# Optimization experiments

Measured on AMD Instinct MI355X. Metric: run time of the kernel, lower is better.

The kernel has to match this reference:

```python
import jax, jax.numpy as jnp
import numpy as np
from jax import lax

B, T, D, L = 64, 512, 1024, 32


def setup_inputs() -> dict:
    key = jax.random.key(0)
    ks = jax.random.split(key, 6)
    embeddings = jax.random.normal(ks[0], (B, T, D), dtype=jnp.float32)
    W = jax.random.normal(ks[1], (L, D), dtype=jnp.float32) * (1.0 / np.sqrt(D))
    b = jnp.zeros((L,), dtype=jnp.float32)
    start_trans = jax.random.normal(ks[2], (L,), dtype=jnp.float32) * 0.1
    end_trans = jax.random.normal(ks[3], (L,), dtype=jnp.float32) * 0.1
    trans = jax.random.normal(ks[4], (L, L), dtype=jnp.float32) * 0.1
    labels = jax.random.randint(ks[5], (B, T), 0, L, dtype=jnp.int32)
    mask = jnp.ones((B, T), dtype=bool)  # torchcrf requires mask[:, 0] == True
    return {"embeddings": embeddings, "W": W, "b": b,
            "start_trans": start_trans, "end_trans": end_trans,
            "trans": trans, "labels": labels, "mask": mask}


def _crf_nll(emissions, labels, mask, start_trans, end_trans, trans):
    # emissions: [B, T, L]; torchcrf works time-first internally.
    em = jnp.transpose(emissions, (1, 0, 2))          # [T, B, L]
    tg = labels.T                                      # [T, B]
    mk_b = mask.T                                      # [T, B] bool
    mk_f = mk_b.astype(emissions.dtype)
    bidx = jnp.arange(em.shape[1])

    # ---- numerator: score of the gold tag path ----
    score0 = start_trans[tg[0]] + em[0, bidx, tg[0]]   # [B]

    def num_step(carry, inp):
        prev_tag, score = carry
        e_t, tag_t, m_b, m_f = inp
        step = trans[prev_tag, tag_t] + e_t[bidx, tag_t]
        score = score + step * m_f
        prev_tag = jnp.where(m_b, tag_t, prev_tag)
        return (prev_tag, score), None

    (last_tag, num), _ = lax.scan(num_step, (tg[0], score0),
                                  (em[1:], tg[1:], mk_b[1:], mk_f[1:]))
    num = num + end_trans[last_tag]

    # ---- denominator: forward algorithm (log partition) ----
    alpha0 = start_trans[None, :] + em[0]              # [B, L]

    def den_step(alpha, inp):
        e_t, m_b = inp
        # alpha[b, i] + trans[i, j] + e_t[b, j] -> logsumexp over i
        nxt = jax.nn.logsumexp(alpha[:, :, None] + trans[None, :, :]
                               + e_t[:, None, :], axis=1)
        alpha = jnp.where(m_b[:, None], nxt, alpha)
        return alpha, None

    alpha, _ = lax.scan(den_step, alpha0, (em[1:], mk_b[1:]))
    den = jax.nn.logsumexp(alpha + end_trans[None, :], axis=1)  # [B]

    llh = num - den                                    # log-likelihood per seq
    return -jnp.mean(llh)                              # reduction='mean', negated


def reference(embeddings, W, b, start_trans, end_trans, trans, labels, mask):
    # dropout is identity at eval time
    emissions = jnp.einsum('btd,ld->btl', embeddings, W) + b  # [B, T, L]
    return _crf_nll(emissions, labels, mask, start_trans, end_trans, trans)
```

## Files before the change

kernel.cpp:

```cpp
#include <hip/hip_runtime.h>
#include <hip/hip_bf16.h>

#define NB 64
#define NT 512
#define ND 1024
#define NL 32
#define SEG 16
#define NSEG 32

typedef __attribute__((ext_vector_type(8)))  short bf16x8;
typedef __attribute__((ext_vector_type(4)))  float f32x4;
typedef __attribute__((ext_vector_type(16))) float f32x16;

__device__ __forceinline__ unsigned short bfh(float x) {
    __hip_bfloat16 h = __float2bfloat16(x);
    return *(unsigned short*)&h;
}
__device__ __forceinline__ float frombf(unsigned short u) {
    return __uint_as_float(((unsigned)u) << 16);
}
__device__ __forceinline__ bf16x8 pack8(float4 x, float4 y) {
    bf16x8 r;
    unsigned short* p = (unsigned short*)&r;
    p[0] = bfh(x.x); p[1] = bfh(x.y); p[2] = bfh(x.z); p[3] = bfh(x.w);
    p[4] = bfh(y.x); p[5] = bfh(y.y); p[6] = bfh(y.z); p[7] = bfh(y.w);
    return r;
}

__global__ __launch_bounds__(256) void wb_kernel(
    const float* __restrict__ W, unsigned short* __restrict__ Wb)
{
    int i = blockIdx.x * 256 + threadIdx.x;
    float4 v = ((const float4*)W)[i];
    ushort4 o;
    o.x = bfh(v.x); o.y = bfh(v.y); o.z = bfh(v.z); o.w = bfh(v.w);
    ((ushort4*)Wb)[i] = o;
}

struct Grp {
    float4 a[4][2];
    bf16x8 b[4][2];
};

__device__ __forceinline__ void load_grp(
    Grp& G, const float* __restrict__ ap,
    const unsigned short* __restrict__ bp0,
    const unsigned short* __restrict__ bp1, int k0)
{
#pragma unroll
    for (int s = 0; s < 4; s++) {
        G.a[s][0] = *(const float4*)(ap + k0 + s * 32);
        G.a[s][1] = *(const float4*)(ap + k0 + s * 32 + 4);
        G.b[s][0] = *(const bf16x8*)(bp0 + k0 + s * 32);
        G.b[s][1] = *(const bf16x8*)(bp1 + k0 + s * 32);
    }
}

__global__ __launch_bounds__(256) void emis_kernel(
    const float* __restrict__ emb,
    const unsigned short* __restrict__ Wb,
    const float* __restrict__ bias,
    float* __restrict__ eme)
{
    const int tid  = threadIdx.x;
    const int wv   = tid >> 6;
    const int lane = tid & 63;
    const int m    = lane & 15;
    const int quad = lane >> 4;
    const int w    = blockIdx.x * 4 + wv;
    const int row  = w * 16 + m;

    const float*          ap  = emb + (size_t)row * ND + quad * 8;
    const unsigned short* bp0 = Wb + (size_t)m * ND + quad * 8;
    const unsigned short* bp1 = Wb + (size_t)(16 + m) * ND + quad * 8;

    f32x4 acc0 = {0.f, 0.f, 0.f, 0.f};
    f32x4 acc1 = {0.f, 0.f, 0.f, 0.f};

    Grp g0, g1;
    load_grp(g0, ap, bp0, bp1, 0);
    load_grp(g1, ap, bp0, bp1, 128);

#pragma unroll
    for (int g = 0; g < 8; g++) {
        Grp& cur = (g & 1) ? g1 : g0;
#pragma unroll
        for (int s = 0; s < 4; s++) {
            bf16x8 af = pack8(cur.a[s][0], cur.a[s][1]);
            acc0 = __builtin_amdgcn_mfma_f32_16x16x32_bf16(af, cur.b[s][0], acc0, 0, 0, 0);
            acc1 = __builtin_amdgcn_mfma_f32_16x16x32_bf16(af, cur.b[s][1], acc1, 0, 0, 0);
        }
        if (g < 6) load_grp(cur, ap, bp0, bp1, (g + 2) * 128);
    }

    const float bl0 = bias[m];
    const float bl1 = bias[16 + m];
#pragma unroll
    for (int r = 0; r < 4; r++) {
        int R = w * 16 + quad * 4 + r;
        float* op = eme + (size_t)R * NL;
        op[m]      = __expf(acc0[r] + bl0);
        op[16 + m] = __expf(acc1[r] + bl1);
    }
}

__global__ __launch_bounds__(64) void seg_kernel(
    const float* __restrict__ eme,
    const float* __restrict__ trans,
    const int*   __restrict__ labels,
    float* __restrict__ Pm,
    int*   __restrict__ exps,
    float* __restrict__ numpart)
{
    const int blk  = blockIdx.x;
    const int b    = blk >> 5;
    const int s    = blk & 31;
    const int lane = threadIdx.x;
    const int col  = lane & 31;
    const int h    = lane >> 5;
    const int t0   = s * SEG;
    const int tstart = (s == 0) ? 1 : t0;

    __shared__ __align__(16) float em_lds[SEG][NL];
    __shared__ __align__(16) unsigned short Thi[2][32][40];
    __shared__ __align__(16) unsigned short Tlo[2][32][40];

    {
        const float* src = eme + ((size_t)b * NT + t0) * NL;
        *(float4*)&((float*)em_lds)[lane * 8]     = *(const float4*)&src[lane * 8];
        *(float4*)&((float*)em_lds)[lane * 8 + 4] = *(const float4*)&src[lane * 8 + 4];
    }
    __syncthreads();

    {
        float npart = 0.f;
        if (lane < SEG) {
            int t = t0 + lane;
            if (t >= 1) {
                int pt = labels[b * NT + t - 1], ct = labels[b * NT + t];
                npart = trans[pt * NL + ct] + __logf(em_lds[lane][ct]);
            }
        }
#pragma unroll
        for (int mk = 32; mk >= 1; mk >>= 1) npart += __shfl_xor(npart, mk, 64);
        if (lane == 0) numpart[b * NSEG + s] = npart;
    }

    float Ecol[16];
#pragma unroll
    for (int j = 0; j < 8; j++) Ecol[j]     = __expf(trans[(8 * h + j) * NL + col]);
#pragma unroll
    for (int j = 0; j < 8; j++) Ecol[8 + j] = __expf(trans[(16 + 8 * h + j) * NL + col]);

    bf16x8 Ah1, Ah2, Al1, Al2;
    {
        const float* emt = em_lds[tstart - t0];
#pragma unroll
        for (int j = 0; j < 8; j++) {
            int k1 = 8 * h + j, k2 = 16 + 8 * h + j;
            float v1 = __expf(trans[col * NL + k1]) * emt[k1];
            float v2 = __expf(trans[col * NL + k2]) * emt[k2];
            unsigned short h1 = bfh(v1), h2 = bfh(v2);
            ((unsigned short*)&Ah1)[j] = h1;
            ((unsigned short*)&Ah2)[j] = h2;
            ((unsigned short*)&Al1)[j] = bfh(v1 - frombf(h1));
            ((unsigned short*)&Al2)[j] = bfh(v2 - frombf(h2));
        }
    }

    int eseg = 0, par = 0;
    const int tlast = t0 + SEG - 1;
    for (int t = tstart + 1; t <= tlast; t++) {
        float emn = em_lds[t - t0][col];
        bf16x8 Bh1, Bh2, Bl1, Bl2;
#pragma unroll
        for (int j = 0; j < 8; j++) {
            float v1 = Ecol[j] * emn;
            float v2 = Ecol[8 + j] * emn;
            unsigned short h1 = bfh(v1), h2 = bfh(v2);
            ((unsigned short*)&Bh1)[j] = h1;
            ((unsigned short*)&Bh2)[j] = h2;
            ((unsigned short*)&Bl1)[j] = bfh(v1 - frombf(h1));
            ((unsigned short*)&Bl2)[j] = bfh(v2 - frombf(h2));
        }

        f32x16 acc;
#pragma unroll
        for (int i = 0; i < 16; i++) acc[i] = 0.f;
        acc = __builtin_amdgcn_mfma_f32_32x32x16_bf16(Ah1, Bh1, acc, 0, 0, 0);
        acc = __builtin_amdgcn_mfma_f32_32x32x16_bf16(Ah2, Bh2, acc, 0, 0, 0);
        acc = __builtin_amdgcn_mfma_f32_32x32x16_bf16(Ah1, Bl1, acc, 0, 0, 0);
        acc = __builtin_amdgcn_mfma_f32_32x32x16_bf16(Ah2, Bl2, acc, 0, 0, 0);
        acc = __builtin_amdgcn_mfma_f32_32x32x16_bf16(Al1, Bh1, acc, 0, 0, 0);
        acc = __builtin_amdgcn_mfma_f32_32x32x16_bf16(Al2, Bh2, acc, 0, 0, 0);

        int bits = __builtin_amdgcn_readlane(__float_as_int(acc[0]), 0);
        int e = (bits >> 23) & 255;
        eseg += e - 127;
        float scale = __uint_as_float((unsigned)(254 - e) << 23);

        if (t < tlast) {
#pragma unroll
            for (int r = 0; r < 16; r++) {
                int row = (r & 3) + 8 * (r >> 2) + 4 * h;
                float v = acc[r] * scale;
                unsigned short hi = bfh(v);
                Thi[par][row][col] = hi;
                Tlo[par][row][col] = bfh(v - frombf(hi));
            }
            __syncthreads();
            Ah1 = *(const bf16x8*)&Thi[par][col][8 * h];
            Ah2 = *(const bf16x8*)&Thi[par][col][16 + 8 * h];
            Al1 = *(const bf16x8*)&Tlo[par][col][8 * h];
            Al2 = *(const bf16x8*)&Tlo[par][col][16 + 8 * h];
            par ^= 1;
        } else {
            float* dst = Pm + ((size_t)(b * NSEG + s) << 10);
#pragma unroll
            for (int r = 0; r < 16; r++) {
                int row = (r & 3) + 8 * (r >> 2) + 4 * h;
                dst[row * 32 + col] = acc[r] * scale;
            }
        }
    }
    if (lane == 0) exps[b * NSEG + s] = eseg;
}

__global__ __launch_bounds__(64) void comb_kernel(
    const float* __restrict__ eme,
    const float* __restrict__ start_trans,
    const float* __restrict__ end_trans,
    const float* __restrict__ Pm,
    const int*   __restrict__ exps,
    const float* __restrict__ numpart,
    const int*   __restrict__ labels,
    float* __restrict__ den_out,
    float* __restrict__ num_out)
{
    const int b    = blockIdx.x;
    const int lane = threadIdx.x;
    const int col  = lane & 31;

    float a = __expf(start_trans[col]) * eme[(size_t)b * NT * NL + col];
    int sexp = 0;
    float sv[32];
#pragma unroll
    for (int i = 0; i < 32; i++)
        sv[i] = __int_as_float(__builtin_amdgcn_readlane(__float_as_int(a), i));

    const float* Pb = Pm + ((size_t)b * NSEG << 10);
    float Pc[32];
#pragma unroll
    for (int i = 0; i < 32; i++) Pc[i] = Pb[i * 32 + col];

    for (int s = 0; s < NSEG; s++) {
        float nb[32];
        if (s + 1 < NSEG) {
            const float* q = Pb + ((s + 1) << 10);
#pragma unroll
            for (int i = 0; i < 32; i++) nb[i] = q[i * 32 + col];
        } else {
#pragma unroll
            for (int i = 0; i < 32; i++) nb[i] = 0.f;
        }

        float p0 = sv[0] * Pc[0], p1 = sv[1] * Pc[1];
        float p2 = sv[2] * Pc[2], p3 = sv[3] * Pc[3];
        float p4 = sv[4] * Pc[4], p5 = sv[5] * Pc[5];
        float p6 = sv[6] * Pc[6], p7 = sv[7] * Pc[7];
#pragma unroll
        for (int i = 8; i < 32; i += 8) {
            p0 = fmaf(sv[i + 0], Pc[i + 0], p0);
            p1 = fmaf(sv[i + 1], Pc[i + 1], p1);
            p2 = fmaf(sv[i + 2], Pc[i + 2], p2);
            p3 = fmaf(sv[i + 3], Pc[i + 3], p3);
            p4 = fmaf(sv[i + 4], Pc[i + 4], p4);
            p5 = fmaf(sv[i + 5], Pc[i + 5], p5);
            p6 = fmaf(sv[i + 6], Pc[i + 6], p6);
            p7 = fmaf(sv[i + 7], Pc[i + 7], p7);
        }
        a = (((p0 + p1) + (p2 + p3)) + ((p4 + p5) + (p6 + p7)));

        int bits = __builtin_amdgcn_readlane(__float_as_int(a), 0);
        int e = (bits >> 23) & 255;
        sexp += e - 127;
        a *= __uint_as_float((unsigned)(254 - e) << 23);

#pragma unroll
        for (int i = 0; i < 32; i++)
            sv[i] = __int_as_float(__builtin_amdgcn_readlane(__float_as_int(a), i));
#pragma unroll
        for (int i = 0; i < 32; i++) Pc[i] = nb[i];
    }

    float sege = (lane < NSEG) ? (float)exps[b * NSEG + lane] : 0.f;
#pragma unroll
    for (int mk = 32; mk >= 1; mk >>= 1) sege += __shfl_xor(sege, mk, 64);

    float x = a * __expf(end_trans[col]);
#pragma unroll
    for (int mk = 16; mk >= 1; mk >>= 1) x += __shfl_xor(x, mk, 32);

    float nsum = (lane < NSEG) ? numpart[b * NSEG + lane] : 0.f;
#pragma unroll
    for (int mk = 32; mk >= 1; mk >>= 1) nsum += __shfl_xor(nsum, mk, 64);

    if (lane == 0) {
        int l0 = labels[b * NT], lT = labels[b * NT + NT - 1];
        num_out[b] = nsum + start_trans[l0]
                   + __logf(eme[(size_t)b * NT * NL + l0]) + end_trans[lT];
        den_out[b] = __logf(x)
                   + 0.69314718055994531f * ((float)sexp + sege);
    }
}

__global__ __launch_bounds__(64) void fin_kernel(
    const float* __restrict__ den, const float* __restrict__ num,
    float* __restrict__ out)
{
    int lane = threadIdx.x;
    float v = den[lane] - num[lane];
#pragma unroll
    for (int mk = 32; mk >= 1; mk >>= 1) v += __shfl_xor(v, mk, 64);
    if (lane == 0) out[0] = v * (1.0f / 64.0f);
}

extern "C" void kernel_launch(void* const* d_in, const int* in_sizes, int n_in,
                              void* d_out, int out_size, void* d_ws, size_t ws_size,
                              hipStream_t stream)
{
    const float* emb    = (const float*)d_in[0];
    const float* W      = (const float*)d_in[1];
    const float* bias   = (const float*)d_in[2];
    const float* st     = (const float*)d_in[3];
    const float* en     = (const float*)d_in[4];
    const float* tr     = (const float*)d_in[5];
    const int*   labels = (const int*)d_in[6];

    char* p = (char*)d_ws;
    float* eme = (float*)p;                  p += (size_t)NB * NT * NL * 4;
    float* Pm  = (float*)p;                  p += (size_t)NB * NSEG * 1024 * 4;
    int*   exps = (int*)p;                   p += NB * NSEG * 4;
    float* nump = (float*)p;                 p += NB * NSEG * 4;
    float* den  = (float*)p;                 p += NB * 4;
    float* num  = (float*)p;                 p += NB * 4;
    unsigned short* Wb = (unsigned short*)p;
    float* out = (float*)d_out;

    wb_kernel  <<<(NL * ND) / 1024, 256, 0, stream>>>(W, Wb);
    emis_kernel<<<(NB * NT) / 64, 256, 0, stream>>>(emb, Wb, bias, eme);
    seg_kernel <<<NB * NSEG, 64, 0, stream>>>(eme, tr, labels, Pm, exps, nump);
    comb_kernel<<<NB, 64, 0, stream>>>(eme, st, en, Pm, exps, nump, labels, den, num);
    fin_kernel <<<1, 64, 0, stream>>>(den, num, out);
}
```

Baseline: 253.0 us.

## Fuse emission GEMM with per-segment CRF transfer-matrix kernel via per-wave LDS

Merges the emission projection kernel and the segment transfer-matrix kernel, so each wave's 16 emission rows (one segment of 16 timesteps) stay in LDS instead of going through global memory. The start-transition term is folded into segment 0's initial matrix, and the combine kernel now starts from a ones vector. Block-level barriers are replaced with per-wave lgkmcnt waits because each wave owns its own LDS slices. This removes one launch and the global round trip of the emissions. The cost is that the seg work now runs with fewer, larger blocks and more LDS per block.

Result: faster. 236.1 us (-6.7%).

```diff
diff --git a/kernel.cpp b/kernel.cpp
--- a/kernel.cpp
+++ b/kernel.cpp
@@ -56,19 +56,31 @@
     }
 }
 
-__global__ __launch_bounds__(256) void emis_kernel(
+__global__ __launch_bounds__(256) void emseg_kernel(
     const float* __restrict__ emb,
     const unsigned short* __restrict__ Wb,
     const float* __restrict__ bias,
-    float* __restrict__ eme)
-{
+    const float* __restrict__ start_trans,
+    const float* __restrict__ trans,
+    const int*   __restrict__ labels,
+    float* __restrict__ Pm,
+    int*   __restrict__ exps,
+    float* __restrict__ numpart)
+{
+    __shared__ float          em_s[4][SEG][36];
+    __shared__ unsigned short Thi_s[4][32][40];
+    __shared__ unsigned short Tlo_s[4][32][40];
+
     const int tid  = threadIdx.x;
     const int wv   = tid >> 6;
     const int lane = tid & 63;
     const int m    = lane & 15;
     const int quad = lane >> 4;
     const int w    = blockIdx.x * 4 + wv;
+    const int b    = w >> 5;
+    const int s    = w & 31;
     const int row  = w * 16 + m;
+    const int t0   = s * SEG;
 
     const float*          ap  = emb + (size_t)row * ND + quad * 8;
     const unsigned short* bp0 = Wb + (size_t)m * ND + quad * 8;
@@ -85,10 +97,10 @@
     for (int g = 0; g < 8; g++) {
         Grp& cur = (g & 1) ? g1 : g0;
 #pragma unroll
-        for (int s = 0; s < 4; s++) {
-            bf16x8 af = pack8(cur.a[s][0], cur.a[s][1]);
-            acc0 = __builtin_amdgcn_mfma_f32_16x16x32_bf16(af, cur.b[s][0], acc0, 0, 0, 0);
-            acc1 = __builtin_amdgcn_mfma_f32_16x16x32_bf16(af, cur.b[s][1], acc1, 0, 0, 0);
+        for (int st = 0; st < 4; st++) {
+            bf16x8 af = pack8(cur.a[st][0], cur.a[st][1]);
+            acc0 = __builtin_amdgcn_mfma_f32_16x16x32_bf16(af, cur.b[st][0], acc0, 0, 0, 0);
+            acc1 = __builtin_amdgcn_mfma_f32_16x16x32_bf16(af, cur.b[st][1], acc1, 0, 0, 0);
         }
         if (g < 6) load_grp(cur, ap, bp0, bp1, (g + 2) * 128);
     }
@@ -97,48 +109,23 @@
     const float bl1 = bias[16 + m];
 #pragma unroll
     for (int r = 0; r < 4; r++) {
-        int R = w * 16 + quad * 4 + r;
-        float* op = eme + (size_t)R * NL;
-        op[m]      = __expf(acc0[r] + bl0);
-        op[16 + m] = __expf(acc1[r] + bl1);
-    }
-}
-
-__global__ __launch_bounds__(64) void seg_kernel(
-    const float* __restrict__ eme,
-    const float* __restrict__ trans,
-    const int*   __restrict__ labels,
-    float* __restrict__ Pm,
-    int*   __restrict__ exps,
-    float* __restrict__ numpart)
-{
-    const int blk  = blockIdx.x;
-    const int b    = blk >> 5;
-    const int s    = blk & 31;
-    const int lane = threadIdx.x;
-    const int col  = lane & 31;
-    const int h    = lane >> 5;
-    const int t0   = s * SEG;
-    const int tstart = (s == 0) ? 1 : t0;
-
-    __shared__ __align__(16) float em_lds[SEG][NL];
-    __shared__ __align__(16) unsigned short Thi[2][32][40];
-    __shared__ __align__(16) unsigned short Tlo[2][32][40];
+        int lt = quad * 4 + r;
+        em_s[wv][lt][m]      = __expf(acc0[r] + bl0);
+        em_s[wv][lt][16 + m] = __expf(acc1[r] + bl1);
+    }
+    asm volatile("s_waitcnt lgkmcnt(0)" ::: "memory");
 
     {
-        const float* src = eme + ((size_t)b * NT + t0) * NL;
-        *(float4*)&((float*)em_lds)[lane * 8]     = *(const float4*)&src[lane * 8];
-        *(float4*)&((float*)em_lds)[lane * 8 + 4] = *(const float4*)&src[lane * 8 + 4];
-    }
-    __syncthreads();
-
-    {
+        const int* lab = labels + b * NT;
         float npart = 0.f;
         if (lane < SEG) {
             int t = t0 + lane;
             if (t >= 1) {
-                int pt = labels[b * NT + t - 1], ct = labels[b * NT + t];
-                npart = trans[pt * NL + ct] + __logf(em_lds[lane][ct]);
+                int pt = lab[t - 1], ct = lab[t];
+                npart = trans[pt * NL + ct] + __logf(em_s[wv][lane][ct]);
+            } else {
+                int c0 = lab[0];
+                npart = start_trans[c0] + __logf(em_s[wv][0][c0]);
             }
         }
 #pragma unroll
@@ -146,6 +133,10 @@
         if (lane == 0) numpart[b * NSEG + s] = npart;
     }
 
+    const int col = lane & 31;
+    const int h   = lane >> 5;
+    const int ls  = (s == 0) ? 1 : 0;
+
     float Ecol[16];
 #pragma unroll
     for (int j = 0; j < 8; j++) Ecol[j]     = __expf(trans[(8 * h + j) * NL + col]);
@@ -154,12 +145,13 @@
 
     bf16x8 Ah1, Ah2, Al1, Al2;
     {
-        const float* emt = em_lds[tstart - t0];
+        float sA = 1.f;
+        if (s == 0) sA = __expf(start_trans[col]) * em_s[wv][0][col];
 #pragma unroll
         for (int j = 0; j < 8; j++) {
             int k1 = 8 * h + j, k2 = 16 + 8 * h + j;
-            float v1 = __expf(trans[col * NL + k1]) * emt[k1];
-            float v2 = __expf(trans[col * NL + k2]) * emt[k2];
+            float v1 = sA * __expf(trans[col * NL + k1]) * em_s[wv][ls][k1];
+            float v2 = sA * __expf(trans[col * NL + k2]) * em_s[wv][ls][k2];
             unsigned short h1 = bfh(v1), h2 = bfh(v2);
             ((unsigned short*)&Ah1)[j] = h1;
             ((unsigned short*)&Ah2)[j] = h2;
@@ -168,10 +160,9 @@
         }
     }
 
-    int eseg = 0, par = 0;
-    const int tlast = t0 + SEG - 1;
-    for (int t = tstart + 1; t <= tlast; t++) {
-        float emn = em_lds[t - t0][col];
+    int eseg = 0;
+    for (int lt = ls + 1; lt < SEG; lt++) {
+        float emn = em_s[wv][lt][col];
         bf16x8 Bh1, Bh2, Bl1, Bl2;
 #pragma unroll
         for (int j = 0; j < 8; j++) {
@@ -199,27 +190,26 @@
         eseg += e - 127;
         float scale = __uint_as_float((unsigned)(254 - e) << 23);
 
-        if (t < tlast) {
+        if (lt < SEG - 1) {
 #pragma unroll
             for (int r = 0; r < 16; r++) {
-                int row = (r & 3) + 8 * (r >> 2) + 4 * h;
+                int rowi = (r & 3) + 8 * (r >> 2) + 4 * h;
                 float v = acc[r] * scale;
                 unsigned short hi = bfh(v);
-                Thi[par][row][col] = hi;
-                Tlo[par][row][col] = bfh(v - frombf(hi));
+                Thi_s[wv][rowi][col] = hi;
+                Tlo_s[wv][rowi][col] = bfh(v - frombf(hi));
             }
-            __syncthreads();
-            Ah1 = *(const bf16x8*)&Thi[par][col][8 * h];
-            Ah2 = *(const bf16x8*)&Thi[par][col][16 + 8 * h];
-            Al1 = *(const bf16x8*)&Tlo[par][col][8 * h];
-            Al2 = *(const bf16x8*)&Tlo[par][col][16 + 8 * h];
-            par ^= 1;
+            asm volatile("s_waitcnt lgkmcnt(0)" ::: "memory");
+            Ah1 = *(const bf16x8*)&Thi_s[wv][col][8 * h];
+            Ah2 = *(const bf16x8*)&Thi_s[wv][col][16 + 8 * h];
+            Al1 = *(const bf16x8*)&Tlo_s[wv][col][8 * h];
+            Al2 = *(const bf16x8*)&Tlo_s[wv][col][16 + 8 * h];
         } else {
             float* dst = Pm + ((size_t)(b * NSEG + s) << 10);
 #pragma unroll
             for (int r = 0; r < 16; r++) {
-                int row = (r & 3) + 8 * (r >> 2) + 4 * h;
-                dst[row * 32 + col] = acc[r] * scale;
+                int rowi = (r & 3) + 8 * (r >> 2) + 4 * h;
+                dst[rowi * 32 + col] = acc[r] * scale;
             }
         }
     }
@@ -227,8 +217,6 @@
 }
 
 __global__ __launch_bounds__(64) void comb_kernel(
-    const float* __restrict__ eme,
-    const float* __restrict__ start_trans,
     const float* __restrict__ end_trans,
     const float* __restrict__ Pm,
     const int*   __restrict__ exps,
@@ -241,18 +229,17 @@
     const int lane = threadIdx.x;
     const int col  = lane & 31;
 
-    float a = __expf(start_trans[col]) * eme[(size_t)b * NT * NL + col];
     int sexp = 0;
     float sv[32];
 #pragma unroll
-    for (int i = 0; i < 32; i++)
-        sv[i] = __int_as_float(__builtin_amdgcn_readlane(__float_as_int(a), i));
+    for (int i = 0; i < 32; i++) sv[i] = 1.0f;
 
     const float* Pb = Pm + ((size_t)b * NSEG << 10);
     float Pc[32];
 #pragma unroll
     for (int i = 0; i < 32; i++) Pc[i] = Pb[i * 32 + col];
 
+    float a = 0.f;
     for (int s = 0; s < NSEG; s++) {
         float nb[32];
         if (s + 1 < NSEG) {
@@ -306,9 +293,8 @@
     for (int mk = 32; mk >= 1; mk >>= 1) nsum += __shfl_xor(nsum, mk, 64);
 
     if (lane == 0) {
-        int l0 = labels[b * NT], lT = labels[b * NT + NT - 1];
-        num_out[b] = nsum + start_trans[l0]
-                   + __logf(eme[(size_t)b * NT * NL + l0]) + end_trans[lT];
+        int lT = labels[b * NT + NT - 1];
+        num_out[b] = nsum + end_trans[lT];
         den_out[b] = __logf(x)
                    + 0.69314718055994531f * ((float)sexp + sege);
     }
@@ -338,7 +324,6 @@
     const int*   labels = (const int*)d_in[6];
 
     char* p = (char*)d_ws;
-    float* eme = (float*)p;                  p += (size_t)NB * NT * NL * 4;
     float* Pm  = (float*)p;                  p += (size_t)NB * NSEG * 1024 * 4;
     int*   exps = (int*)p;                   p += NB * NSEG * 4;
     float* nump = (float*)p;                 p += NB * NSEG * 4;
@@ -347,9 +332,9 @@
     unsigned short* Wb = (unsigned short*)p;
     float* out = (float*)d_out;
 
-    wb_kernel  <<<(NL * ND) / 1024, 256, 0, stream>>>(W, Wb);
-    emis_kernel<<<(NB * NT) / 64, 256, 0, stream>>>(emb, Wb, bias, eme);
-    seg_kernel <<<NB * NSEG, 64, 0, stream>>>(eme, tr, labels, Pm, exps, nump);
-    comb_kernel<<<NB, 64, 0, stream>>>(eme, st, en, Pm, exps, nump, labels, den, num);
-    fin_kernel <<<1, 64, 0, stream>>>(den, num, out);
-}
+    wb_kernel   <<<(NL * ND) / 1024, 256, 0, stream>>>(W, Wb);
+    emseg_kernel<<<(NB * NT) / 64, 256, 0, stream>>>(emb, Wb, bias, st, tr,
+                                                     labels, Pm, exps, nump);
+    comb_kernel <<<NB, 64, 0, stream>>>(en, Pm, exps, nump, labels, den, num);
+    fin_kernel  <<<1, 64, 0, stream>>>(den, num, out);
+}
```
